# Performance work log

Measured on AMD Instinct MI355X. Metric: run time of the kernel, lower is better.

The kernel has to match this reference:

```python
import jax, jax.numpy as jnp
import numpy as np

B, S, WIN, E, H, L = 32, 1024, 1024, 128, 512, 3


def setup_inputs() -> dict:
    key = jax.random.key(0)
    ks = jax.random.split(key, 12)
    rn = lambda k, shape: jax.random.normal(k, shape, dtype=jnp.float32) * 0.05
    z = lambda *shape: jnp.zeros(shape, dtype=jnp.float32)
    return {
        "inputs": jax.random.normal(ks[0], (B, S, WIN), dtype=jnp.float32),
        "mask": jnp.ones((B, S, 1), dtype=jnp.float32),
        "lengths": jnp.full((B,), S, dtype=jnp.int32),  # full-length sequences
        "W_e": rn(ks[1], (E, WIN)), "b_e": z(E),
        "W_a1": rn(ks[2], (E, E)), "b_a1": z(E),
        "W_a2": rn(ks[3], (L, E)), "b_a2": z(L),
        "Wih_e": rn(ks[4], (4 * H, E)), "Whh_e": rn(ks[5], (4 * H, H)),
        "bih_e": z(4 * H), "bhh_e": z(4 * H),
        "enc_h0": z(H), "enc_c0": z(H),
        "Wih_d": rn(ks[6], (4 * H, 1 + H)), "Whh_d": rn(ks[7], (4 * H, H)),
        "bih_d": z(4 * H), "bhh_d": z(4 * H),
        "dec_h0": z(H), "dec_c0": z(H),
        "W_o1": rn(ks[8], (E, H)), "b_o1": z(E),
        "W_o2": rn(ks[9], (1, E)), "b_o2": z(1),
    }


def _cell(gates, c):
    # PyTorch LSTM gate order: i, f, g, o
    i, f, g, o = jnp.split(gates, 4, axis=-1)
    c = jax.nn.sigmoid(f) * c + jax.nn.sigmoid(i) * jnp.tanh(g)
    h = jax.nn.sigmoid(o) * jnp.tanh(c)
    return h, c


def reference(inputs, mask, lengths,
              W_e, b_e, W_a1, b_a1, W_a2, b_a2,
              Wih_e, Whh_e, bih_e, bhh_e, enc_h0, enc_c0,
              Wih_d, Whh_d, bih_d, bhh_d, dec_h0, dec_c0,
              W_o1, b_o1, W_o2, b_o2):
    # embed MLP (dropout inactive at eval)
    embed = jax.nn.relu(jnp.einsum('bsw,ew->bse', inputs, W_e) + b_e)  # (B,S,E)
    # local-attention weights; nn.Softmax(dim=1) normalizes over TIME (faithful)
    a = jax.nn.relu(embed @ W_a1.T + b_a1) @ W_a2.T + b_a2              # (B,S,L)
    attn = jax.nn.softmax(a, axis=1)

    # ---- encoder LSTM (single layer, learned h0/c0) ----
    x_proj = jnp.einsum('bse,ge->bsg', embed, Wih_e) + (bih_e + bhh_e)  # (B,S,4H)
    h0 = jnp.broadcast_to(enc_h0, (B, H))
    c0 = jnp.broadcast_to(enc_c0, (B, H))

    def enc_step(carry, xp):
        h, c = carry
        h, c = _cell(xp + h @ Whh_e.T, c)
        return (h, c), h

    _, enc_hs = jax.lax.scan(enc_step, (h0, c0), jnp.swapaxes(x_proj, 0, 1))
    enc_out = jnp.swapaxes(enc_hs, 0, 1)                                # (B,S,H)
    # pad_packed_sequence zeros positions past each length
    t_idx = jnp.arange(S)[None, :, None]
    enc_out = jnp.where(t_idx < lengths[:, None, None], enc_out, 0.0)

    # ---- convolve: context[b,t] = sum_i attn[b,t,i] * enc_out[b,t-i] ----
    context = attn[..., 0:1] * enc_out
    for i in range(1, L):  # L=3, tiny fixed loop
        shifted = jnp.pad(enc_out[:, :-i, :], ((0, 0), (i, 0), (0, 0)))
        context = context + attn[..., i:i + 1] * shifted

    dh0 = jnp.broadcast_to(dec_h0, (B, H))
    dc0 = jnp.broadcast_to(dec_c0, (B, H))
    p0 = jnp.zeros((B, 1), dtype=inputs.dtype)  # tgt_init = 0.0
    b_d = bih_d + bhh_d

    def dec_step(carry, ctx_t):
        h, c, p = carry
        x = jnp.concatenate([p, ctx_t], axis=1)                         # (B,1+H)
        h, c = _cell(x @ Wih_d.T + h @ Whh_d.T + b_d, c)
        p = jax.nn.relu(h @ W_o1.T + b_o1) @ W_o2.T + b_o2              # (B,1)
        return (h, c, p), p

    _, ps = jax.lax.scan(dec_step, (dh0, dc0, p0), jnp.swapaxes(context, 0, 1))
    predicted = jnp.swapaxes(ps, 0, 1)                                  # (B,S,1)
    return predicted * mask
```

## Files before the change

### kernel.cpp

```cpp
#include <hip/hip_runtime.h>
#include <cstddef>

__device__ __forceinline__ float sigm(float x) { return 1.f / (1.f + __expf(-x)); }
__device__ __forceinline__ float tanh_(float x) { return 1.f - 2.f / (__expf(2.f * x) + 1.f); }

#define AGLD(p)    __hip_atomic_load((p),  __ATOMIC_RELAXED, __HIP_MEMORY_SCOPE_AGENT)
#define AGST(p, v) __hip_atomic_store((p), (v), __ATOMIC_RELAXED, __HIP_MEMORY_SCOPE_AGENT)

#define DOT16(wp, hp, kk) do { \
    float4 w0_ = *(const float4*)((wp) + (kk));      float4 x0_ = *(const float4*)((hp) + (kk)); \
    float4 w1_ = *(const float4*)((wp) + (kk) + 4);  float4 x1_ = *(const float4*)((hp) + (kk) + 4); \
    float4 w2_ = *(const float4*)((wp) + (kk) + 8);  float4 x2_ = *(const float4*)((hp) + (kk) + 8); \
    float4 w3_ = *(const float4*)((wp) + (kk) + 12); float4 x3_ = *(const float4*)((hp) + (kk) + 12); \
    a0 = fmaf(w0_.x, x0_.x, a0); a0 = fmaf(w0_.y, x0_.y, a0); a0 = fmaf(w0_.z, x0_.z, a0); a0 = fmaf(w0_.w, x0_.w, a0); \
    a1 = fmaf(w1_.x, x1_.x, a1); a1 = fmaf(w1_.y, x1_.y, a1); a1 = fmaf(w1_.z, x1_.z, a1); a1 = fmaf(w1_.w, x1_.w, a1); \
    a2 = fmaf(w2_.x, x2_.x, a2); a2 = fmaf(w2_.y, x2_.y, a2); a2 = fmaf(w2_.z, x2_.z, a2); a2 = fmaf(w2_.w, x2_.w, a2); \
    a3 = fmaf(w3_.x, x3_.x, a3); a3 = fmaf(w3_.y, x3_.y, a3); a3 = fmaf(w3_.z, x3_.z, a3); a3 = fmaf(w3_.w, x3_.w, a3); \
  } while (0)

__global__ __launch_bounds__(256) void k_embed(
    const float* __restrict__ inp, const float* __restrict__ We,
    const float* __restrict__ be, float* __restrict__ emb)
{
  __shared__ float sA[32 * 68];
  __shared__ float sW[32 * 132];
  const int tid = threadIdx.x;
  const int b  = blockIdx.x >> 4;
  const int s0 = (blockIdx.x & 15) << 6;
  float acc[4][8];
#pragma unroll
  for (int i = 0; i < 4; ++i)
#pragma unroll
    for (int j = 0; j < 8; ++j) acc[i][j] = 0.f;
  const int m4 = (tid & 15) << 2;
  const int e8 = (tid >> 4) << 3;
  const float* Ab = inp + ((size_t)(b << 10) + s0) * 1024;
  const int ms = tid >> 2, kq = tid & 3;
  const int es = tid >> 1, kq2 = tid & 1;
  for (int k0 = 0; k0 < 1024; k0 += 32) {
    __syncthreads();
    {
      const float* src = Ab + (size_t)ms * 1024 + k0 + (kq << 3);
      float4 v0 = *(const float4*)(src);
      float4 v1 = *(const float4*)(src + 4);
      int kb = kq << 3;
      sA[(kb+0)*68+ms] = v0.x; sA[(kb+1)*68+ms] = v0.y;
      sA[(kb+2)*68+ms] = v0.z; sA[(kb+3)*68+ms] = v0.w;
      sA[(kb+4)*68+ms] = v1.x; sA[(kb+5)*68+ms] = v1.y;
      sA[(kb+6)*68+ms] = v1.z; sA[(kb+7)*68+ms] = v1.w;
    }
    {
      const float* src = We + (size_t)es * 1024 + k0 + (kq2 << 4);
#pragma unroll
      for (int q = 0; q < 4; ++q) {
        float4 v = *(const float4*)(src + (q << 2));
        int kb = (kq2 << 4) + (q << 2);
        sW[(kb+0)*132+es] = v.x; sW[(kb+1)*132+es] = v.y;
        sW[(kb+2)*132+es] = v.z; sW[(kb+3)*132+es] = v.w;
      }
    }
    __syncthreads();
#pragma unroll 4
    for (int kk = 0; kk < 32; ++kk) {
      float4 a4 = *(const float4*)&sA[kk*68 + m4];
      float4 b0 = *(const float4*)&sW[kk*132 + e8];
      float4 b1 = *(const float4*)&sW[kk*132 + e8 + 4];
      float av[4] = {a4.x, a4.y, a4.z, a4.w};
      float bv[8] = {b0.x, b0.y, b0.z, b0.w, b1.x, b1.y, b1.z, b1.w};
#pragma unroll
      for (int i = 0; i < 4; ++i)
#pragma unroll
        for (int j = 0; j < 8; ++j) acc[i][j] = fmaf(av[i], bv[j], acc[i][j]);
    }
  }
#pragma unroll
  for (int i = 0; i < 4; ++i) {
    int s = s0 + m4 + i;
#pragma unroll
    for (int j = 0; j < 8; ++j) {
      float v = acc[i][j] + be[e8 + j];
      emb[((size_t)(s << 5) + b) * 128 + e8 + j] = v > 0.f ? v : 0.f;
    }
  }
}

__global__ __launch_bounds__(256) void k_attn(
    const float* __restrict__ emb, const float* __restrict__ Wa1,
    const float* __restrict__ ba1, const float* __restrict__ Wa2,
    const float* __restrict__ ba2, float* __restrict__ aw)
{
  __shared__ float sE[2 * 128];
  __shared__ float sH[2 * 128];
  const int tid = threadIdx.x;
  const int rs0 = blockIdx.x * 2;
  sE[tid] = emb[(size_t)rs0 * 128 + tid];
  __syncthreads();
  const int half = tid >> 7, j = tid & 127;
  const float* w = Wa1 + j * 128;
  const float* e = sE + half * 128;
  float a0 = 0.f, a1 = 0.f, a2 = 0.f, a3 = 0.f;
  for (int k = 0; k < 128; k += 16) DOT16(w, e, k);
  float h = (a0 + a1) + (a2 + a3) + ba1[j];
  sH[half * 128 + j] = h > 0.f ? h : 0.f;
  __syncthreads();
  if (tid < 6) {
    int hh = tid / 3, l = tid % 3;
    const float* w2 = Wa2 + l * 128;
    const float* hv = sH + hh * 128;
    float s = 0.f;
    for (int k = 0; k < 128; ++k) s = fmaf(w2[k], hv[k], s);
    aw[(size_t)(rs0 + hh) * 3 + l] = s + ba2[l];
  }
}

__global__ __launch_bounds__(256) void k_softmax(float* __restrict__ aw)
{
  __shared__ float red[256];
  const int b = blockIdx.x / 3, l = blockIdx.x % 3;
  const int tid = threadIdx.x;
  float v[4];
#pragma unroll
  for (int i = 0; i < 4; ++i) {
    int s = tid + i * 256;
    v[i] = aw[(size_t)(s * 32 + b) * 3 + l];
  }
  float mx = fmaxf(fmaxf(v[0], v[1]), fmaxf(v[2], v[3]));
  red[tid] = mx;
  __syncthreads();
  for (int off = 128; off > 0; off >>= 1) {
    if (tid < off) red[tid] = fmaxf(red[tid], red[tid + off]);
    __syncthreads();
  }
  mx = red[0];
  __syncthreads();
  float sm = 0.f;
#pragma unroll
  for (int i = 0; i < 4; ++i) sm += __expf(v[i] - mx);
  red[tid] = sm;
  __syncthreads();
  for (int off = 128; off > 0; off >>= 1) {
    if (tid < off) red[tid] += red[tid + off];
    __syncthreads();
  }
  float inv = 1.f / red[0];
#pragma unroll
  for (int i = 0; i < 4; ++i) {
    int s = tid + i * 256;
    aw[(size_t)(s * 32 + b) * 3 + l] = __expf(v[i] - mx) * inv;
  }
}

__global__ __launch_bounds__(256) void k_prep(
    const float* __restrict__ Wih_d,
    const float* __restrict__ bih_e, const float* __restrict__ bhh_e,
    const float* __restrict__ bih_d, const float* __restrict__ bhh_d,
    float* __restrict__ wdpack, float* __restrict__ bsum_e, float* __restrict__ bsum_d)
{
  const int row = blockIdx.x;
  const int tid = threadIdx.x;
  for (int q = tid; q < 516; q += 256) {
    float v = 0.f;
    if (q < 512)      v = Wih_d[(size_t)row * 513 + 1 + q];
    else if (q == 512) v = Wih_d[(size_t)row * 513];
    wdpack[(size_t)row * 516 + q] = v;
  }
  if (tid == 0) {
    bsum_e[row] = bih_e[row] + bhh_e[row];
    bsum_d[row] = bih_d[row] + bhh_d[row];
  }
}

__global__ __launch_bounds__(256) void k_init(
    const float* __restrict__ eh0, const float* __restrict__ dh0,
    const float* __restrict__ bo2,
    float* __restrict__ heb, float* __restrict__ hdb,
    float* __restrict__ out, unsigned* __restrict__ bar)
{
  const int i = blockIdx.x * 256 + threadIdx.x;
  if (i < 16384) {
    int k = i & 511;
    heb[16384 + i] = eh0[k];
    hdb[i] = dh0[k];
  }
  out[i] = bo2[0];
  if (i < 1024) bar[i] = 0u;
}

__device__ __forceinline__ void batchbar(unsigned* cnt, unsigned* flag, unsigned gen)
{
  __builtin_amdgcn_s_waitcnt(0);
  __syncthreads();
  if (threadIdx.x == 0) {
    asm volatile("" ::: "memory");
    unsigned old = __hip_atomic_fetch_add(cnt, 1u, __ATOMIC_RELAXED, __HIP_MEMORY_SCOPE_AGENT);
    if (old == (gen << 3) - 1u)
      AGST(flag, gen);
    while (AGLD(flag) < gen)
      __builtin_amdgcn_s_sleep(1);
    asm volatile("" ::: "memory");
  }
  __syncthreads();
}

__global__ __launch_bounds__(256) void k_persist(
    const float* __restrict__ emb, const float* __restrict__ aw,
    const int* __restrict__ lens,
    const float* __restrict__ Wih_e, const float* __restrict__ Whh_e,
    const float* __restrict__ Whh_d, const float* __restrict__ wdpack,
    const float* __restrict__ bsum_e, const float* __restrict__ bsum_d,
    const float* __restrict__ ec0, const float* __restrict__ dc0,
    const float* __restrict__ Wo1, const float* __restrict__ bo1,
    const float* __restrict__ Wo2, const float* __restrict__ maskp,
    float* __restrict__ heb, float* __restrict__ hdb,
    float* __restrict__ ctxb, float* __restrict__ out,
    unsigned* __restrict__ bar)
{
  __shared__ float sHe[512], sHd[512], sCtx[512], sEmb[128];
  __shared__ float sG[256];
  __shared__ float sPv;
  const int tid = threadIdx.x;
  const int b = blockIdx.x >> 3, s = blockIdx.x & 7;
  const int lane = tid & 63, w = tid >> 6;
  const int r8 = lane >> 3, kg = lane & 7;
  unsigned* cnt  = bar + b * 32;
  unsigned* flag = bar + b * 32 + 16;

  float c_e = 0.f, c_d = 0.f, hm1 = 0.f, hm2 = 0.f;
  int len_b = lens[b];
  if (tid < 64) {
    c_e = ec0[(s << 6) + tid];
    c_d = dc0[(s << 6) + tid];
  }

  unsigned gen = 0;

  for (int t = 0; t < 1024; ++t) {
    {
      const float* hep = heb + (size_t)((t + 1) & 1) * 16384 + b * 512;
      const float* hdp = hdb + b * 512;
      sHe[tid]       = AGLD(hep + tid);
      sHe[tid + 256] = AGLD(hep + tid + 256);
      sHd[tid]       = AGLD(hdp + tid);
      sHd[tid + 256] = AGLD(hdp + tid + 256);
      if (tid < 128) sEmb[tid] = emb[(size_t)(t * 32 + b) * 128 + tid];
    }
    __syncthreads();

    if (t > 0) {
      const int e = (s << 4) + (tid >> 4), ks = tid & 15;
      const float4* wo = (const float4*)(Wo1 + (size_t)e * 512);
      const float4* hd4 = (const float4*)sHd;
      float a0 = 0.f, a1 = 0.f, a2 = 0.f, a3 = 0.f;
#pragma unroll
      for (int j4 = 0; j4 < 8; j4 += 4) {
        float4 wv0 = wo[(j4+0) * 16 + ks], hv0 = hd4[(j4+0) * 16 + ks];
        float4 wv1 = wo[(j4+1) * 16 + ks], hv1 = hd4[(j4+1) * 16 + ks];
        float4 wv2 = wo[(j4+2) * 16 + ks], hv2 = hd4[(j4+2) * 16 + ks];
        float4 wv3 = wo[(j4+3) * 16 + ks], hv3 = hd4[(j4+3) * 16 + ks];
        a0 = fmaf(wv0.x,hv0.x,a0); a0 = fmaf(wv0.y,hv0.y,a0); a0 = fmaf(wv0.z,hv0.z,a0); a0 = fmaf(wv0.w,hv0.w,a0);
        a1 = fmaf(wv1.x,hv1.x,a1); a1 = fmaf(wv1.y,hv1.y,a1); a1 = fmaf(wv1.z,hv1.z,a1); a1 = fmaf(wv1.w,hv1.w,a1);
        a2 = fmaf(wv2.x,hv2.x,a2); a2 = fmaf(wv2.y,hv2.y,a2); a2 = fmaf(wv2.z,hv2.z,a2); a2 = fmaf(wv2.w,hv2.w,a2);
        a3 = fmaf(wv3.x,hv3.x,a3); a3 = fmaf(wv3.y,hv3.y,a3); a3 = fmaf(wv3.z,hv3.z,a3); a3 = fmaf(wv3.w,hv3.w,a3);
      }
      float p_ = (a0 + a1) + (a2 + a3);
      p_ += __shfl_down(p_, 8);
      p_ += __shfl_down(p_, 4);
      p_ += __shfl_down(p_, 2);
      p_ += __shfl_down(p_, 1);
      float contrib = 0.f;
      if (ks == 0) {
        float q = p_ + bo1[e];
        contrib = (q > 0.f ? q : 0.f) * Wo2[e];
      }
      contrib += __shfl(contrib, 16) + __shfl(contrib, 32) + __shfl(contrib, 48);
      if (lane == 0) atomicAdd(&out[b * 1024 + (t - 1)], contrib);
    }

#pragma unroll 2
    for (int pass = 0; pass < 8; ++pass) {
      const int rho = pass * 32 + w * 8 + r8;
      const int grow = ((rho >> 6) << 9) + (s << 6) + (rho & 63);
      const float4* wr = (const float4*)(Whh_e + (size_t)grow * 512);
      const float4* hr = (const float4*)sHe;
      float a0 = 0.f, a1 = 0.f, a2 = 0.f, a3 = 0.f;
#pragma unroll
      for (int kc = 0; kc < 16; kc += 4) {
        float4 w0 = wr[(kc+0)*8+kg], h0 = hr[(kc+0)*8+kg];
        float4 w1 = wr[(kc+1)*8+kg], h1 = hr[(kc+1)*8+kg];
        float4 w2 = wr[(kc+2)*8+kg], h2 = hr[(kc+2)*8+kg];
        float4 w3 = wr[(kc+3)*8+kg], h3 = hr[(kc+3)*8+kg];
        a0 = fmaf(w0.x,h0.x,a0); a0 = fmaf(w0.y,h0.y,a0); a0 = fmaf(w0.z,h0.z,a0); a0 = fmaf(w0.w,h0.w,a0);
        a1 = fmaf(w1.x,h1.x,a1); a1 = fmaf(w1.y,h1.y,a1); a1 = fmaf(w1.z,h1.z,a1); a1 = fmaf(w1.w,h1.w,a1);
        a2 = fmaf(w2.x,h2.x,a2); a2 = fmaf(w2.y,h2.y,a2); a2 = fmaf(w2.z,h2.z,a2); a2 = fmaf(w2.w,h2.w,a2);
        a3 = fmaf(w3.x,h3.x,a3); a3 = fmaf(w3.y,h3.y,a3); a3 = fmaf(w3.z,h3.z,a3); a3 = fmaf(w3.w,h3.w,a3);
      }
      const float4* wx = (const float4*)(Wih_e + (size_t)grow * 128);
      const float4* xr = (const float4*)sEmb;
#pragma unroll
      for (int kc = 0; kc < 4; ++kc) {
        float4 wv = wx[kc*8+kg], xv = xr[kc*8+kg];
        a0 = fmaf(wv.x,xv.x,a0); a1 = fmaf(wv.y,xv.y,a1);
        a2 = fmaf(wv.z,xv.z,a2); a3 = fmaf(wv.w,xv.w,a3);
      }
      float p = (a0 + a1) + (a2 + a3);
      p += __shfl_down(p, 4);
      p += __shfl_down(p, 2);
      p += __shfl_down(p, 1);
      if (kg == 0) sG[rho] = p + bsum_e[grow];
    }
    __syncthreads();

    if (tid < 64) {
      float gi = sG[tid], gf = sG[64 + tid], gg = sG[128 + tid], go = sG[192 + tid];
      c_e = sigm(gf) * c_e + sigm(gi) * tanh_(gg);
      float h = sigm(go) * tanh_(c_e);
      int ci = b * 512 + (s << 6) + tid;
      AGST(&heb[(size_t)(t & 1) * 16384 + ci], h);
      float hmv = (t < len_b) ? h : 0.f;
      const float* at = aw + (size_t)(t * 32 + b) * 3;
      float ctx = at[0] * hmv + at[1] * hm1 + at[2] * hm2;
      hm2 = hm1; hm1 = hmv;
      AGST(&ctxb[ci], ctx);
    }
    batchbar(cnt, flag, ++gen);

    {
      const float* cp = ctxb + b * 512;
      sCtx[tid]       = AGLD(cp + tid);
      sCtx[tid + 256] = AGLD(cp + tid + 256);
      if (tid == 0) sPv = (t == 0) ? 0.f : AGLD(&out[b * 1024 + (t - 1)]);
    }
    __syncthreads();

#pragma unroll 2
    for (int pass = 0; pass < 8; ++pass) {
      const int rho = pass * 32 + w * 8 + r8;
      const int grow = ((rho >> 6) << 9) + (s << 6) + (rho & 63);
      const float4* wh = (const float4*)(Whh_d + (size_t)grow * 512);
      const float4* wc = (const float4*)(wdpack + (size_t)grow * 516);
      const float4* hr = (const float4*)sHd;
      const float4* cr = (const float4*)sCtx;
      float a0 = 0.f, a1 = 0.f, a2 = 0.f, a3 = 0.f;
#pragma unroll
      for (int kc = 0; kc < 16; kc += 2) {
        float4 w0 = wh[(kc+0)*8+kg], h0 = hr[(kc+0)*8+kg];
        float4 w1 = wh[(kc+1)*8+kg], h1 = hr[(kc+1)*8+kg];
        float4 v0 = wc[(kc+0)*8+kg], c0 = cr[(kc+0)*8+kg];
        float4 v1 = wc[(kc+1)*8+kg], c1 = cr[(kc+1)*8+kg];
        a0 = fmaf(w0.x,h0.x,a0); a0 = fmaf(w0.y,h0.y,a0); a0 = fmaf(w0.z,h0.z,a0); a0 = fmaf(w0.w,h0.w,a0);
        a1 = fmaf(w1.x,h1.x,a1); a1 = fmaf(w1.y,h1.y,a1); a1 = fmaf(w1.z,h1.z,a1); a1 = fmaf(w1.w,h1.w,a1);
        a2 = fmaf(v0.x,c0.x,a2); a2 = fmaf(v0.y,c0.y,a2); a2 = fmaf(v0.z,c0.z,a2); a2 = fmaf(v0.w,c0.w,a2);
        a3 = fmaf(v1.x,c1.x,a3); a3 = fmaf(v1.y,c1.y,a3); a3 = fmaf(v1.z,c1.z,a3); a3 = fmaf(v1.w,c1.w,a3);
      }
      float p = (a0 + a1) + (a2 + a3);
      p += __shfl_down(p, 4);
      p += __shfl_down(p, 2);
      p += __shfl_down(p, 1);
      if (kg == 0)
        sG[rho] = p + sPv * wdpack[(size_t)grow * 516 + 512] + bsum_d[grow];
    }
    __syncthreads();

    if (tid < 64) {
      float gi = sG[tid], gf = sG[64 + tid], gg = sG[128 + tid], go = sG[192 + tid];
      c_d = sigm(gf) * c_d + sigm(gi) * tanh_(gg);
      float h = sigm(go) * tanh_(c_d);
      AGST(&hdb[b * 512 + (s << 6) + tid], h);
    }
    batchbar(cnt, flag, ++gen);
  }

  {
    const float* hdp = hdb + b * 512;
    sHd[tid]       = AGLD(hdp + tid);
    sHd[tid + 256] = AGLD(hdp + tid + 256);
  }
  __syncthreads();
  {
    const int e = (s << 4) + (tid >> 4), ks = tid & 15;
    const float4* wo = (const float4*)(Wo1 + (size_t)e * 512);
    const float4* hd4 = (const float4*)sHd;
    float a0 = 0.f, a1 = 0.f, a2 = 0.f, a3 = 0.f;
#pragma unroll
    for (int j4 = 0; j4 < 8; ++j4) {
      float4 wv = wo[j4 * 16 + ks], hv = hd4[j4 * 16 + ks];
      a0 = fmaf(wv.x,hv.x,a0); a1 = fmaf(wv.y,hv.y,a1);
      a2 = fmaf(wv.z,hv.z,a2); a3 = fmaf(wv.w,hv.w,a3);
    }
    float p_ = (a0 + a1) + (a2 + a3);
    p_ += __shfl_down(p_, 8);
    p_ += __shfl_down(p_, 4);
    p_ += __shfl_down(p_, 2);
    p_ += __shfl_down(p_, 1);
    float contrib = 0.f;
    if (ks == 0) {
      float q = p_ + bo1[e];
      contrib = (q > 0.f ? q : 0.f) * Wo2[e];
    }
    contrib += __shfl(contrib, 16) + __shfl(contrib, 32) + __shfl(contrib, 48);
    if (lane == 0) atomicAdd(&out[b * 1024 + 1023], contrib);
  }
  batchbar(cnt, flag, ++gen);

  if (tid < 128) {
    int idx = b * 1024 + (s << 7) + tid;
    float v = AGLD(&out[idx]);
    out[idx] = v * maskp[idx];
  }
}

extern "C" void kernel_launch(void* const* d_in, const int* in_sizes, int n_in,
                              void* d_out, int out_size, void* d_ws, size_t ws_size,
                              hipStream_t stream)
{
  const float* inp   = (const float*)d_in[0];
  const float* maskp = (const float*)d_in[1];
  const int*   lens  = (const int*)d_in[2];
  const float* We    = (const float*)d_in[3];
  const float* be    = (const float*)d_in[4];
  const float* Wa1   = (const float*)d_in[5];
  const float* ba1   = (const float*)d_in[6];
  const float* Wa2   = (const float*)d_in[7];
  const float* ba2   = (const float*)d_in[8];
  const float* Wih_e = (const float*)d_in[9];
  const float* Whh_e = (const float*)d_in[10];
  const float* bih_e = (const float*)d_in[11];
  const float* bhh_e = (const float*)d_in[12];
  const float* eh0   = (const float*)d_in[13];
  const float* ec0   = (const float*)d_in[14];
  const float* Wih_d = (const float*)d_in[15];
  const float* Whh_d = (const float*)d_in[16];
  const float* bih_d = (const float*)d_in[17];
  const float* bhh_d = (const float*)d_in[18];
  const float* dh0   = (const float*)d_in[19];
  const float* dc0   = (const float*)d_in[20];
  const float* Wo1   = (const float*)d_in[21];
  const float* bo1   = (const float*)d_in[22];
  const float* Wo2   = (const float*)d_in[23];
  const float* bo2   = (const float*)d_in[24];

  float* ws     = (float*)d_ws;
  float* emb    = ws;
  float* aw     = emb + 4194304;
  float* heb    = aw + 98304;
  float* hdb    = heb + 32768;
  float* ctxb   = hdb + 16384;
  float* wdpack = ctxb + 16384;
  float* bsum_e = wdpack + 1056768;
  float* bsum_d = bsum_e + 2048;
  unsigned* bar = (unsigned*)(bsum_d + 2048);
  float* outf = (float*)d_out;

  k_embed<<<512, 256, 0, stream>>>(inp, We, be, emb);
  k_attn<<<16384, 256, 0, stream>>>(emb, Wa1, ba1, Wa2, ba2, aw);
  k_softmax<<<96, 256, 0, stream>>>(aw);
  k_prep<<<2048, 256, 0, stream>>>(Wih_d, bih_e, bhh_e, bih_d, bhh_d,
                                   wdpack, bsum_e, bsum_d);
  k_init<<<128, 256, 0, stream>>>(eh0, dh0, bo2, heb, hdb, outf, bar);

  k_persist<<<256, 256, 0, stream>>>(
      emb, aw, lens,
      Wih_e, Whh_e, Whh_d, wdpack, bsum_e, bsum_d,
      ec0, dc0, Wo1, bo1, Wo2, maskp,
      heb, hdb, ctxb, outf, bar);
}
```

Baseline: 25.18 ms.

## Regroup persistent LSTM blocks to share weight rows across eight batches

The persistent kernel now assigns each block 32 gate rows for a group of 8 batches, instead of 256 gate rows for a single batch. Each weight row fetched from memory serves 8 batch dot products, which cuts per-step weight traffic per block. The cost is that synchronisation now spans 64 blocks through a hierarchical counter barrier instead of 8. Each thread also runs a full 512-long serial dot product rather than splitting it across lanes. The output MLP is spread over 16 blocks per group, with a shared-memory reduction before the atomic add.

```diff
diff --git a/kernel.cpp b/kernel.cpp
--- a/kernel.cpp
+++ b/kernel.cpp
@@ -6,6 +6,7 @@
 
 #define AGLD(p)    __hip_atomic_load((p),  __ATOMIC_RELAXED, __HIP_MEMORY_SCOPE_AGENT)
 #define AGST(p, v) __hip_atomic_store((p), (v), __ATOMIC_RELAXED, __HIP_MEMORY_SCOPE_AGENT)
+#define AGADD(p,v) __hip_atomic_fetch_add((p), (v), __ATOMIC_RELAXED, __HIP_MEMORY_SCOPE_AGENT)
 
 #define DOT16(wp, hp, kk) do { \
     float4 w0_ = *(const float4*)((wp) + (kk));      float4 x0_ = *(const float4*)((hp) + (kk)); \
@@ -186,21 +187,49 @@
   if (i < 1024) bar[i] = 0u;
 }
 
-__device__ __forceinline__ void batchbar(unsigned* cnt, unsigned* flag, unsigned gen)
+__device__ __forceinline__ void groupbar(unsigned* gbar, int r, unsigned gen)
 {
   __builtin_amdgcn_s_waitcnt(0);
   __syncthreads();
   if (threadIdx.x == 0) {
     asm volatile("" ::: "memory");
-    unsigned old = __hip_atomic_fetch_add(cnt, 1u, __ATOMIC_RELAXED, __HIP_MEMORY_SCOPE_AGENT);
+    unsigned old = AGADD(gbar + ((r >> 3) << 4), 1u);
     if (old == (gen << 3) - 1u)
-      AGST(flag, gen);
-    while (AGLD(flag) < gen)
+      (void)AGADD(gbar + 128, 1u);
+    while (AGLD(gbar + 128) < (gen << 3))
       __builtin_amdgcn_s_sleep(1);
     asm volatile("" ::: "memory");
   }
   __syncthreads();
 }
+
+#define OUT_DUTY(TI) do { \
+    const int e_ = (r << 3) + (tid >> 5); \
+    const int ob_ = (tid >> 2) & 7; \
+    const int kq_ = tid & 3; \
+    const float* wo_ = Wo1 + (size_t)e_ * 512 + (kq_ << 7); \
+    const float* hd_ = sHd + ob_ * 516 + (kq_ << 7); \
+    float a0 = 0.f, a1 = 0.f, a2 = 0.f, a3 = 0.f; \
+    _Pragma("unroll") \
+    for (int k = 0; k < 128; k += 16) DOT16(wo_, hd_, k); \
+    float p_ = (a0 + a1) + (a2 + a3); \
+    p_ += __shfl_down(p_, 1); \
+    p_ += __shfl_down(p_, 2); \
+    float contrib_ = 0.f; \
+    if (kq_ == 0) { \
+      float q_ = p_ + bo1[e_]; \
+      contrib_ = (q_ > 0.f ? q_ : 0.f) * Wo2[e_]; \
+    } \
+    contrib_ += __shfl_down(contrib_, 32); \
+    { \
+      const int lane_ = tid & 63, wv_ = tid >> 6; \
+      if (lane_ < 32 && (lane_ & 3) == 0) sRed[(wv_ << 3) + (lane_ >> 2)] = contrib_; \
+    } \
+    __syncthreads(); \
+    if (tid < 8) \
+      atomicAdd(&out[(size_t)(gb8 + tid) * 1024 + (TI)], \
+                sRed[tid] + sRed[8 + tid] + sRed[16 + tid] + sRed[24 + tid]); \
+  } while (0)
 
 __global__ __launch_bounds__(256) void k_persist(
     const float* __restrict__ emb, const float* __restrict__ aw,
@@ -215,149 +244,114 @@
     float* __restrict__ ctxb, float* __restrict__ out,
     unsigned* __restrict__ bar)
 {
-  __shared__ float sHe[512], sHd[512], sCtx[512], sEmb[128];
+  __shared__ float sX[8 * 516];
+  __shared__ float sHd[8 * 516];
+  __shared__ float sEmb[8 * 132];
   __shared__ float sG[256];
-  __shared__ float sPv;
+  __shared__ float sP[8];
+  __shared__ float sRed[32];
+
   const int tid = threadIdx.x;
-  const int b = blockIdx.x >> 3, s = blockIdx.x & 7;
-  const int lane = tid & 63, w = tid >> 6;
-  const int r8 = lane >> 3, kg = lane & 7;
-  unsigned* cnt  = bar + b * 32;
-  unsigned* flag = bar + b * 32 + 16;
+  const int g = blockIdx.x >> 6;
+  const int r = blockIdx.x & 63;
+  const int rr = tid >> 3;
+  const int bb = tid & 7;
+  const int grow = ((rr >> 3) << 9) + (r << 3) + (rr & 7);
+  const int gb8 = g << 3;
+
+  unsigned* gbar = bar + g * 160;
+
+  const float be_row = bsum_e[grow];
+  const float bd_row = bsum_d[grow];
+  const float pcoef  = wdpack[(size_t)grow * 516 + 512];
 
   float c_e = 0.f, c_d = 0.f, hm1 = 0.f, hm2 = 0.f;
-  int len_b = lens[b];
+  int len_b = 0;
   if (tid < 64) {
-    c_e = ec0[(s << 6) + tid];
-    c_d = dc0[(s << 6) + tid];
-  }
+    int dim = (r << 3) + (tid >> 3);
+    c_e = ec0[dim];
+    c_d = dc0[dim];
+    len_b = lens[gb8 + (tid & 7)];
+  }
+
+  const float* whe = Whh_e + (size_t)grow * 512;
+  const float* wie = Wih_e + (size_t)grow * 128;
+  const float* whd = Whh_d + (size_t)grow * 512;
+  const float* wdc = wdpack + (size_t)grow * 516;
+  const float* hX  = sX   + bb * 516;
+  const float* hD  = sHd  + bb * 516;
+  const float* hE  = sEmb + bb * 132;
 
   unsigned gen = 0;
 
   for (int t = 0; t < 1024; ++t) {
     {
-      const float* hep = heb + (size_t)((t + 1) & 1) * 16384 + b * 512;
-      const float* hdp = hdb + b * 512;
-      sHe[tid]       = AGLD(hep + tid);
-      sHe[tid + 256] = AGLD(hep + tid + 256);
-      sHd[tid]       = AGLD(hdp + tid);
-      sHd[tid + 256] = AGLD(hdp + tid + 256);
-      if (tid < 128) sEmb[tid] = emb[(size_t)(t * 32 + b) * 128 + tid];
-    }
-    __syncthreads();
-
-    if (t > 0) {
-      const int e = (s << 4) + (tid >> 4), ks = tid & 15;
-      const float4* wo = (const float4*)(Wo1 + (size_t)e * 512);
-      const float4* hd4 = (const float4*)sHd;
+      const float* hep = heb + (size_t)((t + 1) & 1) * 16384 + (size_t)gb8 * 512;
+      const float* hdp = hdb + (size_t)gb8 * 512;
+      float vHe[16], vHd[16];
+#pragma unroll
+      for (int j = 0; j < 16; ++j) {
+        vHe[j] = AGLD(hep + tid + j * 256);
+        vHd[j] = AGLD(hdp + tid + j * 256);
+      }
+      float4 ev = *(const float4*)(emb + (size_t)(t * 32 + gb8 + (tid >> 5)) * 128 + ((tid & 31) << 2));
+#pragma unroll
+      for (int j = 0; j < 16; ++j) {
+        int i = tid + j * 256, bi = i >> 9, kk = i & 511;
+        sX [bi * 516 + kk] = vHe[j];
+        sHd[bi * 516 + kk] = vHd[j];
+      }
+      *(float4*)(sEmb + (tid >> 5) * 132 + ((tid & 31) << 2)) = ev;
+    }
+    __syncthreads();
+
+    {
       float a0 = 0.f, a1 = 0.f, a2 = 0.f, a3 = 0.f;
-#pragma unroll
-      for (int j4 = 0; j4 < 8; j4 += 4) {
-        float4 wv0 = wo[(j4+0) * 16 + ks], hv0 = hd4[(j4+0) * 16 + ks];
-        float4 wv1 = wo[(j4+1) * 16 + ks], hv1 = hd4[(j4+1) * 16 + ks];
-        float4 wv2 = wo[(j4+2) * 16 + ks], hv2 = hd4[(j4+2) * 16 + ks];
-        float4 wv3 = wo[(j4+3) * 16 + ks], hv3 = hd4[(j4+3) * 16 + ks];
-        a0 = fmaf(wv0.x,hv0.x,a0); a0 = fmaf(wv0.y,hv0.y,a0); a0 = fmaf(wv0.z,hv0.z,a0); a0 = fmaf(wv0.w,hv0.w,a0);
-        a1 = fmaf(wv1.x,hv1.x,a1); a1 = fmaf(wv1.y,hv1.y,a1); a1 = fmaf(wv1.z,hv1.z,a1); a1 = fmaf(wv1.w,hv1.w,a1);
-        a2 = fmaf(wv2.x,hv2.x,a2); a2 = fmaf(wv2.y,hv2.y,a2); a2 = fmaf(wv2.z,hv2.z,a2); a2 = fmaf(wv2.w,hv2.w,a2);
-        a3 = fmaf(wv3.x,hv3.x,a3); a3 = fmaf(wv3.y,hv3.y,a3); a3 = fmaf(wv3.z,hv3.z,a3); a3 = fmaf(wv3.w,hv3.w,a3);
-      }
-      float p_ = (a0 + a1) + (a2 + a3);
-      p_ += __shfl_down(p_, 8);
-      p_ += __shfl_down(p_, 4);
-      p_ += __shfl_down(p_, 2);
-      p_ += __shfl_down(p_, 1);
-      float contrib = 0.f;
-      if (ks == 0) {
-        float q = p_ + bo1[e];
-        contrib = (q > 0.f ? q : 0.f) * Wo2[e];
-      }
-      contrib += __shfl(contrib, 16) + __shfl(contrib, 32) + __shfl(contrib, 48);
-      if (lane == 0) atomicAdd(&out[b * 1024 + (t - 1)], contrib);
-    }
-
-#pragma unroll 2
-    for (int pass = 0; pass < 8; ++pass) {
-      const int rho = pass * 32 + w * 8 + r8;
-      const int grow = ((rho >> 6) << 9) + (s << 6) + (rho & 63);
-      const float4* wr = (const float4*)(Whh_e + (size_t)grow * 512);
-      const float4* hr = (const float4*)sHe;
-      float a0 = 0.f, a1 = 0.f, a2 = 0.f, a3 = 0.f;
-#pragma unroll
-      for (int kc = 0; kc < 16; kc += 4) {
-        float4 w0 = wr[(kc+0)*8+kg], h0 = hr[(kc+0)*8+kg];
-        float4 w1 = wr[(kc+1)*8+kg], h1 = hr[(kc+1)*8+kg];
-        float4 w2 = wr[(kc+2)*8+kg], h2 = hr[(kc+2)*8+kg];
-        float4 w3 = wr[(kc+3)*8+kg], h3 = hr[(kc+3)*8+kg];
-        a0 = fmaf(w0.x,h0.x,a0); a0 = fmaf(w0.y,h0.y,a0); a0 = fmaf(w0.z,h0.z,a0); a0 = fmaf(w0.w,h0.w,a0);
-        a1 = fmaf(w1.x,h1.x,a1); a1 = fmaf(w1.y,h1.y,a1); a1 = fmaf(w1.z,h1.z,a1); a1 = fmaf(w1.w,h1.w,a1);
-        a2 = fmaf(w2.x,h2.x,a2); a2 = fmaf(w2.y,h2.y,a2); a2 = fmaf(w2.z,h2.z,a2); a2 = fmaf(w2.w,h2.w,a2);
-        a3 = fmaf(w3.x,h3.x,a3); a3 = fmaf(w3.y,h3.y,a3); a3 = fmaf(w3.z,h3.z,a3); a3 = fmaf(w3.w,h3.w,a3);
-      }
-      const float4* wx = (const float4*)(Wih_e + (size_t)grow * 128);
-      const float4* xr = (const float4*)sEmb;
-#pragma unroll
-      for (int kc = 0; kc < 4; ++kc) {
-        float4 wv = wx[kc*8+kg], xv = xr[kc*8+kg];
-        a0 = fmaf(wv.x,xv.x,a0); a1 = fmaf(wv.y,xv.y,a1);
-        a2 = fmaf(wv.z,xv.z,a2); a3 = fmaf(wv.w,xv.w,a3);
-      }
-      float p = (a0 + a1) + (a2 + a3);
-      p += __shfl_down(p, 4);
-      p += __shfl_down(p, 2);
-      p += __shfl_down(p, 1);
-      if (kg == 0) sG[rho] = p + bsum_e[grow];
-    }
+#pragma unroll 4
+      for (int k = 0; k < 512; k += 16) DOT16(whe, hX, k);
+#pragma unroll
+      for (int k = 0; k < 128; k += 16) DOT16(wie, hE, k);
+      sG[(rr << 3) + bb] = (a0 + a1) + (a2 + a3) + be_row;
+    }
+
+    if (r < 16 && t > 0) { OUT_DUTY(t - 1); }
+
     __syncthreads();
 
     if (tid < 64) {
       float gi = sG[tid], gf = sG[64 + tid], gg = sG[128 + tid], go = sG[192 + tid];
       c_e = sigm(gf) * c_e + sigm(gi) * tanh_(gg);
       float h = sigm(go) * tanh_(c_e);
-      int ci = b * 512 + (s << 6) + tid;
-      AGST(&heb[(size_t)(t & 1) * 16384 + ci], h);
+      int dim = (r << 3) + (tid >> 3);
+      int gb = gb8 + (tid & 7);
+      AGST(&heb[(size_t)(t & 1) * 16384 + (size_t)gb * 512 + dim], h);
       float hmv = (t < len_b) ? h : 0.f;
-      const float* at = aw + (size_t)(t * 32 + b) * 3;
+      const float* at = aw + (size_t)(t * 32 + gb) * 3;
       float ctx = at[0] * hmv + at[1] * hm1 + at[2] * hm2;
       hm2 = hm1; hm1 = hmv;
-      AGST(&ctxb[ci], ctx);
-    }
-    batchbar(cnt, flag, ++gen);
-
-    {
-      const float* cp = ctxb + b * 512;
-      sCtx[tid]       = AGLD(cp + tid);
-      sCtx[tid + 256] = AGLD(cp + tid + 256);
-      if (tid == 0) sPv = (t == 0) ? 0.f : AGLD(&out[b * 1024 + (t - 1)]);
-    }
-    __syncthreads();
-
+      AGST(&ctxb[(size_t)gb * 512 + dim], ctx);
+    }
+    groupbar(gbar, r, ++gen);
+
+    {
+      const float* cp = ctxb + (size_t)gb8 * 512;
+      float vC[16];
+#pragma unroll
+      for (int j = 0; j < 16; ++j) vC[j] = AGLD(cp + tid + j * 256);
+#pragma unroll
+      for (int j = 0; j < 16; ++j) {
+        int i = tid + j * 256, bi = i >> 9, kk = i & 511;
+        sX[bi * 516 + kk] = vC[j];
+      }
+      if (tid < 8) sP[tid] = (t == 0) ? 0.f : AGLD(&out[(size_t)(gb8 + tid) * 1024 + (t - 1)]);
+    }
+    __syncthreads();
+
+    {
+      float a0 = 0.f, a1 = 0.f, a2 = 0.f, a3 = 0.f;
 #pragma unroll 2
-    for (int pass = 0; pass < 8; ++pass) {
-      const int rho = pass * 32 + w * 8 + r8;
-      const int grow = ((rho >> 6) << 9) + (s << 6) + (rho & 63);
-      const float4* wh = (const float4*)(Whh_d + (size_t)grow * 512);
-      const float4* wc = (const float4*)(wdpack + (size_t)grow * 516);
-      const float4* hr = (const float4*)sHd;
-      const float4* cr = (const float4*)sCtx;
-      float a0 = 0.f, a1 = 0.f, a2 = 0.f, a3 = 0.f;
-#pragma unroll
-      for (int kc = 0; kc < 16; kc += 2) {
-        float4 w0 = wh[(kc+0)*8+kg], h0 = hr[(kc+0)*8+kg];
-        float4 w1 = wh[(kc+1)*8+kg], h1 = hr[(kc+1)*8+kg];
-        float4 v0 = wc[(kc+0)*8+kg], c0 = cr[(kc+0)*8+kg];
-        float4 v1 = wc[(kc+1)*8+kg], c1 = cr[(kc+1)*8+kg];
-        a0 = fmaf(w0.x,h0.x,a0); a0 = fmaf(w0.y,h0.y,a0); a0 = fmaf(w0.z,h0.z,a0); a0 = fmaf(w0.w,h0.w,a0);
-        a1 = fmaf(w1.x,h1.x,a1); a1 = fmaf(w1.y,h1.y,a1); a1 = fmaf(w1.z,h1.z,a1); a1 = fmaf(w1.w,h1.w,a1);
-        a2 = fmaf(v0.x,c0.x,a2); a2 = fmaf(v0.y,c0.y,a2); a2 = fmaf(v0.z,c0.z,a2); a2 = fmaf(v0.w,c0.w,a2);
-        a3 = fmaf(v1.x,c1.x,a3); a3 = fmaf(v1.y,c1.y,a3); a3 = fmaf(v1.z,c1.z,a3); a3 = fmaf(v1.w,c1.w,a3);
-      }
-      float p = (a0 + a1) + (a2 + a3);
-      p += __shfl_down(p, 4);
-      p += __shfl_down(p, 2);
-      p += __shfl_down(p, 1);
-      if (kg == 0)
-        sG[rho] = p + sPv * wdpack[(size_t)grow * 516 + 512] + bsum_d[grow];
+      for (int k = 0; k < 512; k += 16) { DOT16(whd, hD, k); DOT16(wdc, hX, k); }
+      sG[(rr << 3) + bb] = (a0 + a1) + (a2 + a3) + pcoef * sP[bb] + bd_row;
     }
     __syncthreads();
 
@@ -365,45 +359,29 @@
       float gi = sG[tid], gf = sG[64 + tid], gg = sG[128 + tid], go = sG[192 + tid];
       c_d = sigm(gf) * c_d + sigm(gi) * tanh_(gg);
       float h = sigm(go) * tanh_(c_d);
-      AGST(&hdb[b * 512 + (s << 6) + tid], h);
-    }
-    batchbar(cnt, flag, ++gen);
-  }
-
-  {
-    const float* hdp = hdb + b * 512;
-    sHd[tid]       = AGLD(hdp + tid);
-    sHd[tid + 256] = AGLD(hdp + tid + 256);
-  }
-  __syncthreads();
-  {
-    const int e = (s << 4) + (tid >> 4), ks = tid & 15;
-    const float4* wo = (const float4*)(Wo1 + (size_t)e * 512);
-    const float4* hd4 = (const float4*)sHd;
-    float a0 = 0.f, a1 = 0.f, a2 = 0.f, a3 = 0.f;
-#pragma unroll
-    for (int j4 = 0; j4 < 8; ++j4) {
-      float4 wv = wo[j4 * 16 + ks], hv = hd4[j4 * 16 + ks];
-      a0 = fmaf(wv.x,hv.x,a0); a1 = fmaf(wv.y,hv.y,a1);
-      a2 = fmaf(wv.z,hv.z,a2); a3 = fmaf(wv.w,hv.w,a3);
-    }
-    float p_ = (a0 + a1) + (a2 + a3);
-    p_ += __shfl_down(p_, 8);
-    p_ += __shfl_down(p_, 4);
-    p_ += __shfl_down(p_, 2);
-    p_ += __shfl_down(p_, 1);
-    float contrib = 0.f;
-    if (ks == 0) {
-      float q = p_ + bo1[e];
-      contrib = (q > 0.f ? q : 0.f) * Wo2[e];
-    }
-    contrib += __shfl(contrib, 16) + __shfl(contrib, 32) + __shfl(contrib, 48);
-    if (lane == 0) atomicAdd(&out[b * 1024 + 1023], contrib);
-  }
-  batchbar(cnt, flag, ++gen);
+      int dim = (r << 3) + (tid >> 3);
+      AGST(&hdb[(size_t)(gb8 + (tid & 7)) * 512 + dim], h);
+    }
+    groupbar(gbar, r, ++gen);
+  }
+
+  if (r < 16) {
+    const float* hdp = hdb + (size_t)gb8 * 512;
+    float vHd[16];
+#pragma unroll
+    for (int j = 0; j < 16; ++j) vHd[j] = AGLD(hdp + tid + j * 256);
+#pragma unroll
+    for (int j = 0; j < 16; ++j) {
+      int i = tid + j * 256, bi = i >> 9, kk = i & 511;
+      sHd[bi * 516 + kk] = vHd[j];
+    }
+    __syncthreads();
+    OUT_DUTY(1023);
+  }
+  groupbar(gbar, r, ++gen);
 
   if (tid < 128) {
-    int idx = b * 1024 + (s << 7) + tid;
+    int idx = blockIdx.x * 128 + tid;
     float v = AGLD(&out[idx]);
     out[idx] = v * maskp[idx];
   }
```

New measurement: 28.56 ms. 1.13x slower.
